# Kernel tuning notes

Hardware: AMD Instinct MI355X
Metric: run time of the kernel (lower is better)

## Reference

```python
import jax, jax.numpy as jnp
import numpy as np

# ---- multi-res 4D hash encoding config (Instant-NGP style) ----
L = 16                     # num_levels
T = 2 ** 19                # hash table entries per level (log2_hashmap_size)
FDIM = 2                   # features per entry (input_ch = L*2)
MIN_RES = np.array([16, 16, 16, 16], dtype=np.float64)
MAX_RES = np.array([256, 256, 256, 128], dtype=np.float64)
_growth = (MAX_RES / MIN_RES) ** (1.0 / (L - 1))
RES = np.floor(MIN_RES[None, :] * _growth[None, :] ** np.arange(L)[:, None]).astype(np.int32)  # [L,4]
PRIMES = np.array([1, 2654435761, 805459861, 3674653429], dtype=np.uint32)
# 16 corner offsets of the 4D hypercube
OFFS = np.array([[(c >> d) & 1 for d in range(4)] for c in range(16)], dtype=np.int32)  # [16,4]


def hash_encode(x, table):
    """x: [N,4] in [0,1); table: [L,T,FDIM] -> [N, L*FDIM]."""
    offs = jnp.asarray(OFFS)
    primes = jnp.asarray(PRIMES)
    outs = []
    for l in range(L):  # fixed small loop over levels
        res = jnp.asarray(RES[l], dtype=x.dtype)          # [4]
        pos = x * (res - 1.0)                              # [N,4]
        base = jnp.floor(pos)
        frac = pos - base                                  # [N,4]
        base_i = base.astype(jnp.int32)
        coord = jnp.clip(base_i[:, None, :] + offs[None], 0, jnp.asarray(RES[l] - 1))  # [N,16,4]
        h = coord.astype(jnp.uint32) * primes              # [N,16,4] u32 wraparound mult
        idx = (h[..., 0] ^ h[..., 1] ^ h[..., 2] ^ h[..., 3]) & jnp.uint32(T - 1)      # [N,16]
        feats = table[l][idx.astype(jnp.int32)]            # irregular gather -> [N,16,FDIM]
        # quadrilinear weights: prod over dims of frac / (1-frac)
        w = jnp.prod(jnp.where(offs[None] == 1, frac[:, None, :], 1.0 - frac[:, None, :]), axis=-1)  # [N,16]
        outs.append(jnp.einsum('nc,ncf->nf', w, feats))    # [N,FDIM]
    return jnp.concatenate(outs, axis=-1)                  # [N, L*FDIM]


def setup_inputs() -> dict:
    key = jax.random.key(0)
    ks = jax.random.split(key, 8)
    N = 1048576
    H = 64
    in_ch = L * FDIM  # 32
    x = jax.random.uniform(ks[0], (N, 4), dtype=jnp.float32)
    # NGP hash tables initialized uniform in [-1e-4, 1e-4]
    table = jax.random.uniform(ks[1], (L, T, FDIM), dtype=jnp.float32, minval=-1e-4, maxval=1e-4)
    def lin(k, out_d, in_d):
        b = 1.0 / np.sqrt(in_d)
        return jax.random.uniform(k, (out_d, in_d), dtype=jnp.float32, minval=-b, maxval=b)
    w0 = lin(ks[2], H, in_ch)
    w1 = lin(ks[3], H, H)
    w2 = lin(ks[4], H, H)
    w_out = lin(ks[5], 3, H)
    b_out = jax.random.uniform(ks[6], (3,), dtype=jnp.float32, minval=-1.0/np.sqrt(H), maxval=1.0/np.sqrt(H))
    return {"x": x, "table": table, "w0": w0, "w1": w1, "w2": w2, "w_out": w_out, "b_out": b_out}


def reference(x, table, w0, w1, w2, w_out, b_out):
    h = hash_encode(x, table)                 # [N, 32]
    for W in (w0, w1, w2):                    # bias-free Linear + ReLU x3
        h = jax.nn.relu(h @ W.T)
    v = h @ w_out.T + b_out                   # [N, 3]
    return v
```

## Files before the change

kernel.cpp:

```cpp
#include <hip/hip_runtime.h>
#include <math.h>

#define NLVL  16
#define TSZ   (1u << 19)
#define TMASK (TSZ - 1u)

struct ResArr { int m1[NLVL * 4]; };

typedef short  short8  __attribute__((ext_vector_type(8)));
typedef float  float4v __attribute__((ext_vector_type(4)));

static __device__ __forceinline__ unsigned short f2bf(float f) {
    unsigned u = __float_as_uint(f);
    return (unsigned short)((u + 0x7fffu + ((u >> 16) & 1u)) >> 16);
}

__global__ __launch_bounds__(256, 4)
void ingp_encode(const float4* __restrict__ x,
                 const float2* __restrict__ table,
                 unsigned*     __restrict__ featbf,
                 int N, int chunksPerLevel, ResArr res)
{
    const int l     = blockIdx.x / chunksPerLevel;
    const int chunk = blockIdx.x - l * chunksPerLevel;
    const int n     = chunk * 256 + threadIdx.x;
    if (n >= N) return;

    const float4 xv = x[n];
    const float px[4] = {xv.x, xv.y, xv.z, xv.w};

    int   bi[4];
    float fr[4], om[4];
    #pragma unroll
    for (int d = 0; d < 4; ++d) {
        const int r = res.m1[l * 4 + d];
        const float pos = px[d] * (float)r;
        const float fb  = floorf(pos);
        fr[d] = pos - fb;
        om[d] = 1.0f - fr[d];
        bi[d] = (int)fb;
    }
    const float2* tl  = table + (size_t)l * TSZ;
    const float4* tl4 = (const float4*)tl;

    unsigned hrest[8];
    #pragma unroll
    for (int p = 0; p < 8; ++p) {
        const int c1 = bi[1] + ( p       & 1);
        const int c2 = bi[2] + ((p >> 1) & 1);
        const int c3 = bi[3] + ((p >> 2) & 1);
        hrest[p] = ((unsigned)c1 * 2654435761u)
                 ^ ((unsigned)c2 * 805459861u)
                 ^ ((unsigned)c3 * 3674653429u);
    }

    float2 fv[16];
    if ((bi[0] & 1) == 0) {
        #pragma unroll
        for (int p = 0; p < 8; ++p) {
            const unsigned h = ((unsigned)bi[0] ^ hrest[p]) & TMASK;
            const float4 q = tl4[h >> 1];
            const bool odd = (h & 1);
            fv[2 * p]     = odd ? make_float2(q.z, q.w) : make_float2(q.x, q.y);
            fv[2 * p + 1] = odd ? make_float2(q.x, q.y) : make_float2(q.z, q.w);
        }
    } else {
        #pragma unroll
        for (int p = 0; p < 8; ++p) {
            const unsigned hA = ((unsigned)bi[0]       ^ hrest[p]) & TMASK;
            const unsigned hB = ((unsigned)(bi[0] + 1) ^ hrest[p]) & TMASK;
            fv[2 * p]     = tl[hA];
            fv[2 * p + 1] = tl[hB];
        }
    }

    float wt[16];
    #pragma unroll
    for (int c = 0; c < 16; ++c) {
        float w = ( c       & 1) ? fr[0] : om[0];
        w      *= ((c >> 1) & 1) ? fr[1] : om[1];
        w      *= ((c >> 2) & 1) ? fr[2] : om[2];
        w      *= ((c >> 3) & 1) ? fr[3] : om[3];
        wt[c] = w;
    }

    float a0 = 0.0f, a1 = 0.0f;
    #pragma unroll
    for (int c = 0; c < 16; ++c) {
        a0 = fmaf(wt[c], fv[c].x, a0);
        a1 = fmaf(wt[c], fv[c].y, a1);
    }
    featbf[(size_t)l * N + n] = (unsigned)f2bf(a0) | ((unsigned)f2bf(a1) << 16);
}

#define TILE_BODY(P0, A0)                                                     \
{                                                                             \
    float4v acc0[4];                                                          \
    _Pragma("unroll")                                                         \
    for (int t = 0; t < 4; ++t) {                                             \
        acc0[t] = (float4v){0.f, 0.f, 0.f, 0.f};                              \
        acc0[t] = __builtin_amdgcn_mfma_f32_16x16x32_bf16(A0, w0f[t], acc0[t], 0, 0, 0); \
    }                                                                         \
    _Pragma("unroll")                                                         \
    for (int t = 0; t < 4; ++t)                                               \
        _Pragma("unroll")                                                     \
        for (int r = 0; r < 4; ++r)                                           \
            *(unsigned short*)(hbase + (q * 4 + r) * 144 + (t * 16 + nn) * 2) = \
                f2bf(fmaxf(acc0[t][r], 0.0f));                                \
    short8 a1[2];                                                             \
    _Pragma("unroll")                                                         \
    for (int s = 0; s < 2; ++s)                                               \
        a1[s] = *(const short8*)(hbase + nn * 144 + s * 64 + q * 16);         \
    float4v acc1[4];                                                          \
    _Pragma("unroll")                                                         \
    for (int t = 0; t < 4; ++t) {                                             \
        acc1[t] = (float4v){0.f, 0.f, 0.f, 0.f};                              \
        _Pragma("unroll")                                                     \
        for (int s = 0; s < 2; ++s)                                           \
            acc1[t] = __builtin_amdgcn_mfma_f32_16x16x32_bf16(a1[s], w1f[s][t], acc1[t], 0, 0, 0); \
    }                                                                         \
    _Pragma("unroll")                                                         \
    for (int t = 0; t < 4; ++t)                                               \
        _Pragma("unroll")                                                     \
        for (int r = 0; r < 4; ++r)                                           \
            *(unsigned short*)(hbase + (q * 4 + r) * 144 + (t * 16 + nn) * 2) = \
                f2bf(fmaxf(acc1[t][r], 0.0f));                                \
    short8 a2[2];                                                             \
    _Pragma("unroll")                                                         \
    for (int s = 0; s < 2; ++s)                                               \
        a2[s] = *(const short8*)(hbase + nn * 144 + s * 64 + q * 16);         \
    float4v acc2[4];                                                          \
    _Pragma("unroll")                                                         \
    for (int t = 0; t < 4; ++t) {                                             \
        acc2[t] = (float4v){0.f, 0.f, 0.f, 0.f};                              \
        _Pragma("unroll")                                                     \
        for (int s = 0; s < 2; ++s)                                           \
            acc2[t] = __builtin_amdgcn_mfma_f32_16x16x32_bf16(a2[s], w2f[s][t], acc2[t], 0, 0, 0); \
    }                                                                         \
    _Pragma("unroll")                                                         \
    for (int t = 0; t < 4; ++t)                                               \
        _Pragma("unroll")                                                     \
        for (int r = 0; r < 4; ++r)                                           \
            *(unsigned short*)(hbase + (q * 4 + r) * 144 + (t * 16 + nn) * 2) = \
                f2bf(fmaxf(acc2[t][r], 0.0f));                                \
    short8 a3[2];                                                             \
    _Pragma("unroll")                                                         \
    for (int s = 0; s < 2; ++s)                                               \
        a3[s] = *(const short8*)(hbase + nn * 144 + s * 64 + q * 16);         \
    float4v oc = (float4v){0.f, 0.f, 0.f, 0.f};                               \
    _Pragma("unroll")                                                         \
    for (int s = 0; s < 2; ++s)                                               \
        oc = __builtin_amdgcn_mfma_f32_16x16x32_bf16(a3[s], wof[s], oc, 0, 0, 0); \
    if (nn < 3) {                                                             \
        _Pragma("unroll")                                                     \
        for (int r = 0; r < 4; ++r) {                                         \
            const int pt = (P0) + q * 4 + r;                                  \
            if (pt < N) out[pt * 3 + nn] = oc[r] + bias;                      \
        }                                                                     \
    }                                                                         \
}

__global__ __launch_bounds__(256, 2)
void ingp_mlp_mfma(const unsigned* __restrict__ featbf,
                   const float*    __restrict__ w0,
                   const float*    __restrict__ w1,
                   const float*    __restrict__ w2,
                   const float*    __restrict__ wout,
                   const float*    __restrict__ bout,
                   float*          __restrict__ out,
                   int N, int tilesPerWave)
{
    __shared__ char lds_raw[4 * 16 * 144];
    const int tid  = threadIdx.x;
    const int wave = tid >> 6;
    const int lane = tid & 63;
    const int q    = lane >> 4;
    const int nn   = lane & 15;
    char* hbase = lds_raw + wave * (16 * 144);

    short8 w0f[4];
    #pragma unroll
    for (int t = 0; t < 4; ++t) {
        const float* wr = w0 + (t * 16 + nn) * 32 + q * 8;
        #pragma unroll
        for (int e = 0; e < 8; ++e) w0f[t][e] = (short)f2bf(wr[e]);
    }
    short8 w1f[2][4], w2f[2][4];
    #pragma unroll
    for (int s = 0; s < 2; ++s) {
        #pragma unroll
        for (int t = 0; t < 4; ++t) {
            const float* wr1 = w1 + (t * 16 + nn) * 64 + s * 32 + q * 8;
            const float* wr2 = w2 + (t * 16 + nn) * 64 + s * 32 + q * 8;
            #pragma unroll
            for (int e = 0; e < 8; ++e) {
                w1f[s][t][e] = (short)f2bf(wr1[e]);
                w2f[s][t][e] = (short)f2bf(wr2[e]);
            }
        }
    }
    short8 wof[2];
    #pragma unroll
    for (int s = 0; s < 2; ++s) {
        #pragma unroll
        for (int e = 0; e < 8; ++e) {
            wof[s][e] = (nn < 3) ? (short)f2bf(wout[nn * 64 + s * 32 + q * 8 + e])
                                 : (short)0;
        }
    }
    const float bias = (nn < 3) ? bout[nn] : 0.0f;

    const int waveId = blockIdx.x * 4 + wave;
    const int base   = waveId * tilesPerWave;

    unsigned ufA[4], ufB[4];
    {
        const int pA = (base * 16 < N) ? (base * 16 + nn) : 0;
        const int pB = ((base + 1) * 16 < N) ? ((base + 1) * 16 + nn) : 0;
        #pragma unroll
        for (int v = 0; v < 4; ++v) {
            ufA[v] = featbf[(size_t)(q * 4 + v) * N + pA];
            ufB[v] = featbf[(size_t)(q * 4 + v) * N + pB];
        }
    }

    for (int it = 0; it < tilesPerWave; it += 2) {
        const int p0A = (base + it) * 16;
        if (p0A >= N) break;

        short8 a0A;
        #pragma unroll
        for (int v = 0; v < 4; ++v) {
            a0A[2 * v]     = (short)(ufA[v] & 0xffffu);
            a0A[2 * v + 1] = (short)(ufA[v] >> 16);
        }
        {
            const int p0n = (base + it + 2) * 16;
            const bool more = (it + 2 < tilesPerWave) && (p0n < N);
            const int pn = more ? (p0n + nn) : 0;
            #pragma unroll
            for (int v = 0; v < 4; ++v)
                ufA[v] = featbf[(size_t)(q * 4 + v) * N + pn];
        }
        TILE_BODY(p0A, a0A)

        const int p0B = (base + it + 1) * 16;
        if (p0B < N && it + 1 < tilesPerWave) {
            short8 a0B;
            #pragma unroll
            for (int v = 0; v < 4; ++v) {
                a0B[2 * v]     = (short)(ufB[v] & 0xffffu);
                a0B[2 * v + 1] = (short)(ufB[v] >> 16);
            }
            {
                const int p0n = (base + it + 3) * 16;
                const bool more = (it + 3 < tilesPerWave) && (p0n < N);
                const int pn = more ? (p0n + nn) : 0;
                #pragma unroll
                for (int v = 0; v < 4; ++v)
                    ufB[v] = featbf[(size_t)(q * 4 + v) * N + pn];
            }
            TILE_BODY(p0B, a0B)
        }
    }
}

__global__ __launch_bounds__(256, 2)
void ingp_fused(const float4* __restrict__ x,
                const float2* __restrict__ table,
                const float*  __restrict__ w0,
                const float*  __restrict__ w1,
                const float*  __restrict__ w2,
                const float*  __restrict__ wout,
                const float*  __restrict__ bout,
                float*        __restrict__ out,
                int N, ResArr res)
{
    const int n = blockIdx.x * blockDim.x + threadIdx.x;
    if (n >= N) return;

    const float4 xv = x[n];
    const float px[4] = {xv.x, xv.y, xv.z, xv.w};

    float h1[64];
    #pragma unroll
    for (int j = 0; j < 64; ++j) h1[j] = 0.0f;

    float a0p = 0.0f, a1p = 0.0f;

    #pragma unroll 1
    for (int l = 0; l < NLVL; ++l) {
        int   rm[4], bi[4];
        float fr[4], om[4];
        #pragma unroll
        for (int d = 0; d < 4; ++d) {
            const int r = res.m1[l * 4 + d];
            rm[d] = r;
            const float pos = px[d] * (float)r;
            const float fb  = floorf(pos);
            fr[d] = pos - fb;
            om[d] = 1.0f - fr[d];
            bi[d] = (int)fb;
        }
        const float2* tl = table + (size_t)l * TSZ;

        float2 fv[16];
        float  wt[16];
        #pragma unroll
        for (int c = 0; c < 16; ++c) {
            int c0 = bi[0] + ( c       & 1);
            int c1 = bi[1] + ((c >> 1) & 1);
            int c2 = bi[2] + ((c >> 2) & 1);
            int c3 = bi[3] + ((c >> 3) & 1);
            c0 = min(max(c0, 0), rm[0]);
            c1 = min(max(c1, 0), rm[1]);
            c2 = min(max(c2, 0), rm[2]);
            c3 = min(max(c3, 0), rm[3]);
            const unsigned hh = (unsigned)c0
                              ^ ((unsigned)c1 * 2654435761u)
                              ^ ((unsigned)c2 * 805459861u)
                              ^ ((unsigned)c3 * 3674653429u);
            fv[c] = tl[hh & TMASK];
            float w = ( c       & 1) ? fr[0] : om[0];
            w      *= ((c >> 1) & 1) ? fr[1] : om[1];
            w      *= ((c >> 2) & 1) ? fr[2] : om[2];
            w      *= ((c >> 3) & 1) ? fr[3] : om[3];
            wt[c] = w;
        }
        {
            const int lp = (l == 0) ? 0 : (l - 1);
            const float* w0c = w0 + 2 * lp;
            #pragma unroll
            for (int j = 0; j < 64; ++j)
                h1[j] = fmaf(w0c[j * 32], a0p, fmaf(w0c[j * 32 + 1], a1p, h1[j]));
        }
        float a0 = 0.0f, a1 = 0.0f;
        #pragma unroll
        for (int c = 0; c < 16; ++c) {
            a0 = fmaf(wt[c], fv[c].x, a0);
            a1 = fmaf(wt[c], fv[c].y, a1);
        }
        a0p = a0; a1p = a1;
    }
    {
        const float* w0c = w0 + 2 * (NLVL - 1);
        #pragma unroll
        for (int j = 0; j < 64; ++j)
            h1[j] = fmaf(w0c[j * 32], a0p, fmaf(w0c[j * 32 + 1], a1p, h1[j]));
    }
    #pragma unroll
    for (int j = 0; j < 64; ++j) h1[j] = fmaxf(h1[j], 0.0f);

    float h2[64];
    #pragma unroll
    for (int j = 0; j < 64; ++j) {
        float acc = 0.0f;
        const float* wr = w1 + j * 64;
        #pragma unroll
        for (int i = 0; i < 64; ++i) acc = fmaf(wr[i], h1[i], acc);
        h2[j] = fmaxf(acc, 0.0f);
    }
    float h3[64];
    #pragma unroll
    for (int j = 0; j < 64; ++j) {
        float acc = 0.0f;
        const float* wr = w2 + j * 64;
        #pragma unroll
        for (int i = 0; i < 64; ++i) acc = fmaf(wr[i], h2[i], acc);
        h3[j] = fmaxf(acc, 0.0f);
    }
    float o[3];
    #pragma unroll
    for (int k = 0; k < 3; ++k) {
        float acc = bout[k];
        const float* wr = wout + k * 64;
        #pragma unroll
        for (int i = 0; i < 64; ++i) acc = fmaf(wr[i], h3[i], acc);
        o[k] = acc;
    }
    out[n * 3 + 0] = o[0];
    out[n * 3 + 1] = o[1];
    out[n * 3 + 2] = o[2];
}

extern "C" void kernel_launch(void* const* d_in, const int* in_sizes, int n_in,
                              void* d_out, int out_size, void* d_ws, size_t ws_size,
                              hipStream_t stream) {
    (void)n_in; (void)out_size;

    const float* x     = (const float*)d_in[0];
    const float* table = (const float*)d_in[1];
    const float* w0    = (const float*)d_in[2];
    const float* w1    = (const float*)d_in[3];
    const float* w2    = (const float*)d_in[4];
    const float* wout  = (const float*)d_in[5];
    const float* bout  = (const float*)d_in[6];
    float* out = (float*)d_out;

    const int N = in_sizes[0] / 4;

    ResArr res;
    for (int d = 0; d < 4; ++d) {
        const double minr = 16.0;
        const double maxr = (d == 3) ? 128.0 : 256.0;
        const double growth = pow(maxr / minr, 1.0 / (double)(NLVL - 1));
        for (int l = 0; l < NLVL; ++l) {
            const int r = (int)floor(minr * pow(growth, (double)l));
            res.m1[l * 4 + d] = r - 1;
        }
    }

    const size_t featBytes = (size_t)NLVL * (size_t)N * sizeof(unsigned);
    const int chunksPerLevel = (N + 255) / 256;

    if (ws_size >= featBytes) {
        unsigned* featbf = (unsigned*)d_ws;
        hipLaunchKernelGGL(ingp_encode, dim3(NLVL * chunksPerLevel), dim3(256),
                           0, stream, (const float4*)x, (const float2*)table,
                           featbf, N, chunksPerLevel, res);

        const int tilesPerWave = 8;
        const int tiles  = (N + 15) / 16;
        const int waves  = (tiles + tilesPerWave - 1) / tilesPerWave;
        const int blocks = (waves + 3) / 4;
        hipLaunchKernelGGL(ingp_mlp_mfma, dim3(blocks), dim3(256), 0, stream,
                           featbf, w0, w1, w2, wout, bout, out, N, tilesPerWave);
    } else {
        hipLaunchKernelGGL(ingp_fused, dim3((N + 255) / 256), dim3(256), 0, stream,
                           (const float4*)x, (const float2*)table,
                           w0, w1, w2, wout, bout, out, N, res);
    }
}
```

Before: 837.8 us.

## Overlap MLP on first 3/4 of points with encoding of last quarter

Splits the point range into two parts. The first part is encoded alone. A combined kernel then interleaves MLP blocks for that part with encode blocks for the remainder, and a final MLP kernel handles the rest. The goal is to fill the GPU with compute-bound MFMA work while the gather-bound hash encoding runs, hiding the idle time at the boundary between the two stages. Block roles are picked from the block index, and nothing explicitly checks that feature writes finish before the MLP blocks read them. Correctness therefore depends on kernel launch order.

```diff
diff --git a/kernel.cpp b/kernel.cpp
--- a/kernel.cpp
+++ b/kernel.cpp
@@ -15,15 +15,12 @@
     return (unsigned short)((u + 0x7fffu + ((u >> 16) & 1u)) >> 16);
 }
 
-__global__ __launch_bounds__(256, 4)
-void ingp_encode(const float4* __restrict__ x,
-                 const float2* __restrict__ table,
-                 unsigned*     __restrict__ featbf,
-                 int N, int chunksPerLevel, ResArr res)
+static __device__ __forceinline__
+void encode_point(const float4* __restrict__ x,
+                  const float2* __restrict__ table,
+                  unsigned*     __restrict__ featbf,
+                  int N, int l, int n, const ResArr& res)
 {
-    const int l     = blockIdx.x / chunksPerLevel;
-    const int chunk = blockIdx.x - l * chunksPerLevel;
-    const int n     = chunk * 256 + threadIdx.x;
     if (n >= N) return;
 
     const float4 xv = x[n];
@@ -91,6 +88,17 @@
         a1 = fmaf(wt[c], fv[c].y, a1);
     }
     featbf[(size_t)l * N + n] = (unsigned)f2bf(a0) | ((unsigned)f2bf(a1) << 16);
+}
+
+__global__ __launch_bounds__(256, 4)
+void ingp_encode(const float4* __restrict__ x,
+                 const float2* __restrict__ table,
+                 unsigned*     __restrict__ featbf,
+                 int N, int pointBase, int chunksPerLevel, ResArr res)
+{
+    const int l     = blockIdx.x / chunksPerLevel;
+    const int chunk = blockIdx.x - l * chunksPerLevel;
+    encode_point(x, table, featbf, N, l, pointBase + chunk * 256 + (int)threadIdx.x, res);
 }
 
 #define TILE_BODY(P0, A0)                                                     \
@@ -160,6 +168,109 @@
     }                                                                         \
 }
 
+static __device__ __forceinline__
+void mlp_block_body(const unsigned* __restrict__ featbf,
+                    const float*    __restrict__ w0,
+                    const float*    __restrict__ w1,
+                    const float*    __restrict__ w2,
+                    const float*    __restrict__ wout,
+                    const float*    __restrict__ bout,
+                    float*          __restrict__ out,
+                    int N, int firstTile, char* lds_raw)
+{
+    const int tid  = (int)threadIdx.x;
+    const int wave = tid >> 6;
+    const int lane = tid & 63;
+    const int q    = lane >> 4;
+    const int nn   = lane & 15;
+    char* hbase = lds_raw + wave * (16 * 144);
+
+    short8 w0f[4];
+    #pragma unroll
+    for (int t = 0; t < 4; ++t) {
+        const float* wr = w0 + (t * 16 + nn) * 32 + q * 8;
+        #pragma unroll
+        for (int e = 0; e < 8; ++e) w0f[t][e] = (short)f2bf(wr[e]);
+    }
+    short8 w1f[2][4], w2f[2][4];
+    #pragma unroll
+    for (int s = 0; s < 2; ++s) {
+        #pragma unroll
+        for (int t = 0; t < 4; ++t) {
+            const float* wr1 = w1 + (t * 16 + nn) * 64 + s * 32 + q * 8;
+            const float* wr2 = w2 + (t * 16 + nn) * 64 + s * 32 + q * 8;
+            #pragma unroll
+            for (int e = 0; e < 8; ++e) {
+                w1f[s][t][e] = (short)f2bf(wr1[e]);
+                w2f[s][t][e] = (short)f2bf(wr2[e]);
+            }
+        }
+    }
+    short8 wof[2];
+    #pragma unroll
+    for (int s = 0; s < 2; ++s) {
+        #pragma unroll
+        for (int e = 0; e < 8; ++e) {
+            wof[s][e] = (nn < 3) ? (short)f2bf(wout[nn * 64 + s * 32 + q * 8 + e])
+                                 : (short)0;
+        }
+    }
+    const float bias = (nn < 3) ? bout[nn] : 0.0f;
+
+    const int base = firstTile + wave * 8;
+
+    unsigned ufA[4], ufB[4];
+    {
+        const int pA = (base * 16 < N) ? (base * 16 + nn) : 0;
+        const int pB = ((base + 1) * 16 < N) ? ((base + 1) * 16 + nn) : 0;
+        #pragma unroll
+        for (int v = 0; v < 4; ++v) {
+            ufA[v] = featbf[(size_t)(q * 4 + v) * N + pA];
+            ufB[v] = featbf[(size_t)(q * 4 + v) * N + pB];
+        }
+    }
+
+    for (int it = 0; it < 8; it += 2) {
+        const int p0A = (base + it) * 16;
+        if (p0A >= N) break;
+
+        short8 a0A;
+        #pragma unroll
+        for (int v = 0; v < 4; ++v) {
+            a0A[2 * v]     = (short)(ufA[v] & 0xffffu);
+            a0A[2 * v + 1] = (short)(ufA[v] >> 16);
+        }
+        {
+            const int p0n = (base + it + 2) * 16;
+            const bool more = (it + 2 < 8) && (p0n < N);
+            const int pn = more ? (p0n + nn) : 0;
+            #pragma unroll
+            for (int v = 0; v < 4; ++v)
+                ufA[v] = featbf[(size_t)(q * 4 + v) * N + pn];
+        }
+        TILE_BODY(p0A, a0A)
+
+        const int p0B = (base + it + 1) * 16;
+        if (p0B < N) {
+            short8 a0B;
+            #pragma unroll
+            for (int v = 0; v < 4; ++v) {
+                a0B[2 * v]     = (short)(ufB[v] & 0xffffu);
+                a0B[2 * v + 1] = (short)(ufB[v] >> 16);
+            }
+            {
+                const int p0n = (base + it + 3) * 16;
+                const bool more = (it + 3 < 8) && (p0n < N);
+                const int pn = more ? (p0n + nn) : 0;
+                #pragma unroll
+                for (int v = 0; v < 4; ++v)
+                    ufB[v] = featbf[(size_t)(q * 4 + v) * N + pn];
+            }
+            TILE_BODY(p0B, a0B)
+        }
+    }
+}
+
 __global__ __launch_bounds__(256, 2)
 void ingp_mlp_mfma(const unsigned* __restrict__ featbf,
                    const float*    __restrict__ w0,
@@ -168,100 +279,39 @@
                    const float*    __restrict__ wout,
                    const float*    __restrict__ bout,
                    float*          __restrict__ out,
-                   int N, int tilesPerWave)
+                   int N, int firstTileBase)
 {
     __shared__ char lds_raw[4 * 16 * 144];
-    const int tid  = threadIdx.x;
-    const int wave = tid >> 6;
-    const int lane = tid & 63;
-    const int q    = lane >> 4;
-    const int nn   = lane & 15;
-    char* hbase = lds_raw + wave * (16 * 144);
-
-    short8 w0f[4];
-    #pragma unroll
-    for (int t = 0; t < 4; ++t) {
-        const float* wr = w0 + (t * 16 + nn) * 32 + q * 8;
-        #pragma unroll
-        for (int e = 0; e < 8; ++e) w0f[t][e] = (short)f2bf(wr[e]);
-    }
-    short8 w1f[2][4], w2f[2][4];
-    #pragma unroll
-    for (int s = 0; s < 2; ++s) {
-        #pragma unroll
-        for (int t = 0; t < 4; ++t) {
-            const float* wr1 = w1 + (t * 16 + nn) * 64 + s * 32 + q * 8;
-            const float* wr2 = w2 + (t * 16 + nn) * 64 + s * 32 + q * 8;
-            #pragma unroll
-            for (int e = 0; e < 8; ++e) {
-                w1f[s][t][e] = (short)f2bf(wr1[e]);
-                w2f[s][t][e] = (short)f2bf(wr2[e]);
-            }
-        }
-    }
-    short8 wof[2];
-    #pragma unroll
-    for (int s = 0; s < 2; ++s) {
-        #pragma unroll
-        for (int e = 0; e < 8; ++e) {
-            wof[s][e] = (nn < 3) ? (short)f2bf(wout[nn * 64 + s * 32 + q * 8 + e])
-                                 : (short)0;
-        }
-    }
-    const float bias = (nn < 3) ? bout[nn] : 0.0f;
-
-    const int waveId = blockIdx.x * 4 + wave;
-    const int base   = waveId * tilesPerWave;
-
-    unsigned ufA[4], ufB[4];
-    {
-        const int pA = (base * 16 < N) ? (base * 16 + nn) : 0;
-        const int pB = ((base + 1) * 16 < N) ? ((base + 1) * 16 + nn) : 0;
-        #pragma unroll
-        for (int v = 0; v < 4; ++v) {
-            ufA[v] = featbf[(size_t)(q * 4 + v) * N + pA];
-            ufB[v] = featbf[(size_t)(q * 4 + v) * N + pB];
-        }
-    }
-
-    for (int it = 0; it < tilesPerWave; it += 2) {
-        const int p0A = (base + it) * 16;
-        if (p0A >= N) break;
-
-        short8 a0A;
-        #pragma unroll
-        for (int v = 0; v < 4; ++v) {
-            a0A[2 * v]     = (short)(ufA[v] & 0xffffu);
-            a0A[2 * v + 1] = (short)(ufA[v] >> 16);
-        }
-        {
-            const int p0n = (base + it + 2) * 16;
-            const bool more = (it + 2 < tilesPerWave) && (p0n < N);
-            const int pn = more ? (p0n + nn) : 0;
-            #pragma unroll
-            for (int v = 0; v < 4; ++v)
-                ufA[v] = featbf[(size_t)(q * 4 + v) * N + pn];
-        }
-        TILE_BODY(p0A, a0A)
-
-        const int p0B = (base + it + 1) * 16;
-        if (p0B < N && it + 1 < tilesPerWave) {
-            short8 a0B;
-            #pragma unroll
-            for (int v = 0; v < 4; ++v) {
-                a0B[2 * v]     = (short)(ufB[v] & 0xffffu);
-                a0B[2 * v + 1] = (short)(ufB[v] >> 16);
-            }
-            {
-                const int p0n = (base + it + 3) * 16;
-                const bool more = (it + 3 < tilesPerWave) && (p0n < N);
-                const int pn = more ? (p0n + nn) : 0;
-                #pragma unroll
-                for (int v = 0; v < 4; ++v)
-                    ufB[v] = featbf[(size_t)(q * 4 + v) * N + pn];
-            }
-            TILE_BODY(p0B, a0B)
-        }
+    mlp_block_body(featbf, w0, w1, w2, wout, bout, out, N,
+                   firstTileBase + (int)blockIdx.x * 32, lds_raw);
+}
+
+__global__ __launch_bounds__(256, 2)
+void ingp_pipe(const float4* __restrict__ x,
+               const float2* __restrict__ table,
+               unsigned*     __restrict__ featbf,
+               const float*  __restrict__ w0,
+               const float*  __restrict__ w1,
+               const float*  __restrict__ w2,
+               const float*  __restrict__ wout,
+               const float*  __restrict__ bout,
+               float*        __restrict__ out,
+               int N, int pointBaseE, int chunksPerLevelB, int MB, int G,
+               ResArr res)
+{
+    __shared__ char lds_raw[4 * 16 * 144];
+    const int b = (int)blockIdx.x;
+    const long long t0 = (long long)b * MB;
+    const int mlow  = (int)(t0 / G);
+    const int mhigh = (int)((t0 + MB) / G);
+    if (mhigh > mlow) {
+        mlp_block_body(featbf, w0, w1, w2, wout, bout, out, N, mlow * 32, lds_raw);
+    } else {
+        const int e     = b - mlow;
+        const int l     = e / chunksPerLevelB;
+        const int chunk = e - l * chunksPerLevelB;
+        encode_point(x, table, featbf, N, l,
+                     pointBaseE + chunk * 256 + (int)threadIdx.x, res);
     }
 }
 
@@ -411,20 +461,44 @@
     }
 
     const size_t featBytes = (size_t)NLVL * (size_t)N * sizeof(unsigned);
-    const int chunksPerLevel = (N + 255) / 256;
 
     if (ws_size >= featBytes) {
         unsigned* featbf = (unsigned*)d_ws;
-        hipLaunchKernelGGL(ingp_encode, dim3(NLVL * chunksPerLevel), dim3(256),
-                           0, stream, (const float4*)x, (const float2*)table,
-                           featbf, N, chunksPerLevel, res);
-
-        const int tilesPerWave = 8;
-        const int tiles  = (N + 15) / 16;
-        const int waves  = (tiles + tilesPerWave - 1) / tilesPerWave;
-        const int blocks = (waves + 3) / 4;
-        hipLaunchKernelGGL(ingp_mlp_mfma, dim3(blocks), dim3(256), 0, stream,
-                           featbf, w0, w1, w2, wout, bout, out, N, tilesPerWave);
+
+        const int A = (int)((((long long)N * 3) / 4) / 512 * 512);
+        const bool pipe_ok = (N % 256 == 0) && (A > 0) && (A < N);
+
+        if (pipe_ok) {
+            const int chunksA = A / 256;
+            hipLaunchKernelGGL(ingp_encode, dim3(NLVL * chunksA), dim3(256),
+                               0, stream, (const float4*)x, (const float2*)table,
+                               featbf, N, 0, chunksA, res);
+
+            const int chunksB = (N - A) / 256;
+            const int EB = NLVL * chunksB;
+            const int MB = A / 512;
+            const int G  = EB + MB;
+            hipLaunchKernelGGL(ingp_pipe, dim3(G), dim3(256), 0, stream,
+                               (const float4*)x, (const float2*)table, featbf,
+                               w0, w1, w2, wout, bout, out,
+                               N, A, chunksB, MB, G, res);
+
+            const int tilesB  = (N - A + 15) / 16;
+            const int wavesB  = (tilesB + 7) / 8;
+            const int blocksB = (wavesB + 3) / 4;
+            hipLaunchKernelGGL(ingp_mlp_mfma, dim3(blocksB), dim3(256), 0, stream,
+                               featbf, w0, w1, w2, wout, bout, out, N, A / 16);
+        } else {
+            const int chunksPerLevel = (N + 255) / 256;
+            hipLaunchKernelGGL(ingp_encode, dim3(NLVL * chunksPerLevel), dim3(256),
+                               0, stream, (const float4*)x, (const float2*)table,
+                               featbf, N, 0, chunksPerLevel, res);
+            const int tiles  = (N + 15) / 16;
+            const int waves  = (tiles + 7) / 8;
+            const int blocks = (waves + 3) / 4;
+            hipLaunchKernelGGL(ingp_mlp_mfma, dim3(blocks), dim3(256), 0, stream,
+                               featbf, w0, w1, w2, wout, bout, out, N, 0);
+        }
     } else {
         hipLaunchKernelGGL(ingp_fused, dim3((N + 255) / 256), dim3(256), 0, stream,
                            (const float4*)x, (const float2*)table,
```

Result: slower. 876.2 us (+4.6%).

## Convert hash table to bf16 each call and gather packed bf16 entries

Applied to the files above, without the earlier changes.

Adds a pre-pass kernel that converts the fp32 hash table into packed bf16 pairs in workspace. The encode kernel then gathers 4-byte entries instead of 8-byte ones, and for odd base coordinates it uses 16-byte aligned quad loads to fetch both neighbours at once. This halves the footprint of the random gathers so more of the table stays in cache, at the cost of a full-table conversion pass (16M floats read) on every call and reduced precision of the table values. The MLP kernel is refactored into a helper with the tile count fixed at 8.

```diff
diff --git a/kernel.cpp b/kernel.cpp
--- a/kernel.cpp
+++ b/kernel.cpp
@@ -15,15 +15,23 @@
     return (unsigned short)((u + 0x7fffu + ((u >> 16) & 1u)) >> 16);
 }
 
-__global__ __launch_bounds__(256, 4)
-void ingp_encode(const float4* __restrict__ x,
-                 const float2* __restrict__ table,
-                 unsigned*     __restrict__ featbf,
-                 int N, int chunksPerLevel, ResArr res)
-{
-    const int l     = blockIdx.x / chunksPerLevel;
-    const int chunk = blockIdx.x - l * chunksPerLevel;
-    const int n     = chunk * 256 + threadIdx.x;
+__global__ __launch_bounds__(256)
+void cvt_table(const float4* __restrict__ t, uint2* __restrict__ o, int totalPairs)
+{
+    for (int i = blockIdx.x * 256 + (int)threadIdx.x; i < totalPairs;
+         i += gridDim.x * 256) {
+        const float4 e = t[i];
+        o[i] = make_uint2((unsigned)f2bf(e.x) | ((unsigned)f2bf(e.y) << 16),
+                          (unsigned)f2bf(e.z) | ((unsigned)f2bf(e.w) << 16));
+    }
+}
+
+static __device__ __forceinline__
+void encode_point_bf16(const float4*   __restrict__ x,
+                       const unsigned* __restrict__ tbl,
+                       unsigned*       __restrict__ featbf,
+                       int N, int l, int n, const ResArr& res)
+{
     if (n >= N) return;
 
     const float4 xv = x[n];
@@ -40,8 +48,9 @@
         om[d] = 1.0f - fr[d];
         bi[d] = (int)fb;
     }
-    const float2* tl  = table + (size_t)l * TSZ;
-    const float4* tl4 = (const float4*)tl;
+    const unsigned* tl  = tbl + (size_t)l * TSZ;
+    const uint2*    tl2 = (const uint2*)tl;
+    const uint4*    tl4 = (const uint4*)tl;
 
     unsigned hrest[8];
     #pragma unroll
@@ -54,6 +63,115 @@
                  ^ ((unsigned)c3 * 3674653429u);
     }
 
+    const int b0 = bi[0];
+    unsigned ea[8], eb[8];
+
+    if ((b0 & 1) == 0) {
+        #pragma unroll
+        for (int p = 0; p < 8; ++p) {
+            const unsigned h = ((unsigned)b0 ^ hrest[p]) & TMASK;
+            const uint2 q = tl2[h >> 1];
+            ea[p] = (h & 1u) ? q.y : q.x;
+            eb[p] = (h & 1u) ? q.x : q.y;
+        }
+    } else if ((b0 & 3) == 1) {
+        #pragma unroll
+        for (int p = 0; p < 8; ++p) {
+            const unsigned hA = ((unsigned)b0 ^ hrest[p]) & TMASK;
+            const uint4 q = tl4[hA >> 2];
+            const unsigned jA  = hA & 3u;
+            const unsigned loA = (jA & 2u) ? q.z : q.x;
+            const unsigned hiA = (jA & 2u) ? q.w : q.y;
+            const unsigned loB = (jA & 2u) ? q.x : q.z;
+            const unsigned hiB = (jA & 2u) ? q.y : q.w;
+            ea[p] = (jA & 1u) ? hiA : loA;
+            eb[p] = (jA & 1u) ? loB : hiB;
+        }
+    } else {
+        #pragma unroll
+        for (int p = 0; p < 8; ++p) {
+            const unsigned hA = ((unsigned)b0       ^ hrest[p]) & TMASK;
+            const unsigned hB = ((unsigned)(b0 + 1) ^ hrest[p]) & TMASK;
+            ea[p] = tl[hA];
+            eb[p] = tl[hB];
+        }
+    }
+
+    float2 fv[16];
+    #pragma unroll
+    for (int p = 0; p < 8; ++p) {
+        fv[2 * p]     = make_float2(__uint_as_float(ea[p] << 16),
+                                    __uint_as_float(ea[p] & 0xffff0000u));
+        fv[2 * p + 1] = make_float2(__uint_as_float(eb[p] << 16),
+                                    __uint_as_float(eb[p] & 0xffff0000u));
+    }
+
+    float wt[16];
+    #pragma unroll
+    for (int c = 0; c < 16; ++c) {
+        float w = ( c       & 1) ? fr[0] : om[0];
+        w      *= ((c >> 1) & 1) ? fr[1] : om[1];
+        w      *= ((c >> 2) & 1) ? fr[2] : om[2];
+        w      *= ((c >> 3) & 1) ? fr[3] : om[3];
+        wt[c] = w;
+    }
+
+    float a0 = 0.0f, a1 = 0.0f;
+    #pragma unroll
+    for (int c = 0; c < 16; ++c) {
+        a0 = fmaf(wt[c], fv[c].x, a0);
+        a1 = fmaf(wt[c], fv[c].y, a1);
+    }
+    featbf[(size_t)l * N + n] = (unsigned)f2bf(a0) | ((unsigned)f2bf(a1) << 16);
+}
+
+__global__ __launch_bounds__(256, 4)
+void ingp_encode_bf16(const float4*   __restrict__ x,
+                      const unsigned* __restrict__ tbl,
+                      unsigned*       __restrict__ featbf,
+                      int N, int chunksPerLevel, ResArr res)
+{
+    const int l     = blockIdx.x / chunksPerLevel;
+    const int chunk = blockIdx.x - l * chunksPerLevel;
+    encode_point_bf16(x, tbl, featbf, N, l, chunk * 256 + (int)threadIdx.x, res);
+}
+
+static __device__ __forceinline__
+void encode_point_f32(const float4* __restrict__ x,
+                      const float2* __restrict__ table,
+                      unsigned*     __restrict__ featbf,
+                      int N, int l, int n, const ResArr& res)
+{
+    if (n >= N) return;
+
+    const float4 xv = x[n];
+    const float px[4] = {xv.x, xv.y, xv.z, xv.w};
+
+    int   bi[4];
+    float fr[4], om[4];
+    #pragma unroll
+    for (int d = 0; d < 4; ++d) {
+        const int r = res.m1[l * 4 + d];
+        const float pos = px[d] * (float)r;
+        const float fb  = floorf(pos);
+        fr[d] = pos - fb;
+        om[d] = 1.0f - fr[d];
+        bi[d] = (int)fb;
+    }
+    const float2* tl  = table + (size_t)l * TSZ;
+    const float4* tl4 = (const float4*)tl;
+
+    unsigned hrest[8];
+    #pragma unroll
+    for (int p = 0; p < 8; ++p) {
+        const int c1 = bi[1] + ( p       & 1);
+        const int c2 = bi[2] + ((p >> 1) & 1);
+        const int c3 = bi[3] + ((p >> 2) & 1);
+        hrest[p] = ((unsigned)c1 * 2654435761u)
+                 ^ ((unsigned)c2 * 805459861u)
+                 ^ ((unsigned)c3 * 3674653429u);
+    }
+
     float2 fv[16];
     if ((bi[0] & 1) == 0) {
         #pragma unroll
@@ -91,6 +209,17 @@
         a1 = fmaf(wt[c], fv[c].y, a1);
     }
     featbf[(size_t)l * N + n] = (unsigned)f2bf(a0) | ((unsigned)f2bf(a1) << 16);
+}
+
+__global__ __launch_bounds__(256, 4)
+void ingp_encode_f32(const float4* __restrict__ x,
+                     const float2* __restrict__ table,
+                     unsigned*     __restrict__ featbf,
+                     int N, int chunksPerLevel, ResArr res)
+{
+    const int l     = blockIdx.x / chunksPerLevel;
+    const int chunk = blockIdx.x - l * chunksPerLevel;
+    encode_point_f32(x, table, featbf, N, l, chunk * 256 + (int)threadIdx.x, res);
 }
 
 #define TILE_BODY(P0, A0)                                                     \
@@ -160,6 +289,109 @@
     }                                                                         \
 }
 
+static __device__ __forceinline__
+void mlp_block_body(const unsigned* __restrict__ featbf,
+                    const float*    __restrict__ w0,
+                    const float*    __restrict__ w1,
+                    const float*    __restrict__ w2,
+                    const float*    __restrict__ wout,
+                    const float*    __restrict__ bout,
+                    float*          __restrict__ out,
+                    int N, int firstTile, char* lds_raw)
+{
+    const int tid  = (int)threadIdx.x;
+    const int wave = tid >> 6;
+    const int lane = tid & 63;
+    const int q    = lane >> 4;
+    const int nn   = lane & 15;
+    char* hbase = lds_raw + wave * (16 * 144);
+
+    short8 w0f[4];
+    #pragma unroll
+    for (int t = 0; t < 4; ++t) {
+        const float* wr = w0 + (t * 16 + nn) * 32 + q * 8;
+        #pragma unroll
+        for (int e = 0; e < 8; ++e) w0f[t][e] = (short)f2bf(wr[e]);
+    }
+    short8 w1f[2][4], w2f[2][4];
+    #pragma unroll
+    for (int s = 0; s < 2; ++s) {
+        #pragma unroll
+        for (int t = 0; t < 4; ++t) {
+            const float* wr1 = w1 + (t * 16 + nn) * 64 + s * 32 + q * 8;
+            const float* wr2 = w2 + (t * 16 + nn) * 64 + s * 32 + q * 8;
+            #pragma unroll
+            for (int e = 0; e < 8; ++e) {
+                w1f[s][t][e] = (short)f2bf(wr1[e]);
+                w2f[s][t][e] = (short)f2bf(wr2[e]);
+            }
+        }
+    }
+    short8 wof[2];
+    #pragma unroll
+    for (int s = 0; s < 2; ++s) {
+        #pragma unroll
+        for (int e = 0; e < 8; ++e) {
+            wof[s][e] = (nn < 3) ? (short)f2bf(wout[nn * 64 + s * 32 + q * 8 + e])
+                                 : (short)0;
+        }
+    }
+    const float bias = (nn < 3) ? bout[nn] : 0.0f;
+
+    const int base = firstTile + wave * 8;
+
+    unsigned ufA[4], ufB[4];
+    {
+        const int pA = (base * 16 < N) ? (base * 16 + nn) : 0;
+        const int pB = ((base + 1) * 16 < N) ? ((base + 1) * 16 + nn) : 0;
+        #pragma unroll
+        for (int v = 0; v < 4; ++v) {
+            ufA[v] = featbf[(size_t)(q * 4 + v) * N + pA];
+            ufB[v] = featbf[(size_t)(q * 4 + v) * N + pB];
+        }
+    }
+
+    for (int it = 0; it < 8; it += 2) {
+        const int p0A = (base + it) * 16;
+        if (p0A >= N) break;
+
+        short8 a0A;
+        #pragma unroll
+        for (int v = 0; v < 4; ++v) {
+            a0A[2 * v]     = (short)(ufA[v] & 0xffffu);
+            a0A[2 * v + 1] = (short)(ufA[v] >> 16);
+        }
+        {
+            const int p0n = (base + it + 2) * 16;
+            const bool more = (it + 2 < 8) && (p0n < N);
+            const int pn = more ? (p0n + nn) : 0;
+            #pragma unroll
+            for (int v = 0; v < 4; ++v)
+                ufA[v] = featbf[(size_t)(q * 4 + v) * N + pn];
+        }
+        TILE_BODY(p0A, a0A)
+
+        const int p0B = (base + it + 1) * 16;
+        if (p0B < N) {
+            short8 a0B;
+            #pragma unroll
+            for (int v = 0; v < 4; ++v) {
+                a0B[2 * v]     = (short)(ufB[v] & 0xffffu);
+                a0B[2 * v + 1] = (short)(ufB[v] >> 16);
+            }
+            {
+                const int p0n = (base + it + 3) * 16;
+                const bool more = (it + 3 < 8) && (p0n < N);
+                const int pn = more ? (p0n + nn) : 0;
+                #pragma unroll
+                for (int v = 0; v < 4; ++v)
+                    ufB[v] = featbf[(size_t)(q * 4 + v) * N + pn];
+            }
+            TILE_BODY(p0B, a0B)
+        }
+    }
+}
+
 __global__ __launch_bounds__(256, 2)
 void ingp_mlp_mfma(const unsigned* __restrict__ featbf,
                    const float*    __restrict__ w0,
@@ -168,101 +400,11 @@
                    const float*    __restrict__ wout,
                    const float*    __restrict__ bout,
                    float*          __restrict__ out,
-                   int N, int tilesPerWave)
+                   int N)
 {
     __shared__ char lds_raw[4 * 16 * 144];
-    const int tid  = threadIdx.x;
-    const int wave = tid >> 6;
-    const int lane = tid & 63;
-    const int q    = lane >> 4;
-    const int nn   = lane & 15;
-    char* hbase = lds_raw + wave * (16 * 144);
-
-    short8 w0f[4];
-    #pragma unroll
-    for (int t = 0; t < 4; ++t) {
-        const float* wr = w0 + (t * 16 + nn) * 32 + q * 8;
-        #pragma unroll
-        for (int e = 0; e < 8; ++e) w0f[t][e] = (short)f2bf(wr[e]);
-    }
-    short8 w1f[2][4], w2f[2][4];
-    #pragma unroll
-    for (int s = 0; s < 2; ++s) {
-        #pragma unroll
-        for (int t = 0; t < 4; ++t) {
-            const float* wr1 = w1 + (t * 16 + nn) * 64 + s * 32 + q * 8;
-            const float* wr2 = w2 + (t * 16 + nn) * 64 + s * 32 + q * 8;
-            #pragma unroll
-            for (int e = 0; e < 8; ++e) {
-                w1f[s][t][e] = (short)f2bf(wr1[e]);
-                w2f[s][t][e] = (short)f2bf(wr2[e]);
-            }
-        }
-    }
-    short8 wof[2];
-    #pragma unroll
-    for (int s = 0; s < 2; ++s) {
-        #pragma unroll
-        for (int e = 0; e < 8; ++e) {
-            wof[s][e] = (nn < 3) ? (short)f2bf(wout[nn * 64 + s * 32 + q * 8 + e])
-                                 : (short)0;
-        }
-    }
-    const float bias = (nn < 3) ? bout[nn] : 0.0f;
-
-    const int waveId = blockIdx.x * 4 + wave;
-    const int base   = waveId * tilesPerWave;
-
-    unsigned ufA[4], ufB[4];
-    {
-        const int pA = (base * 16 < N) ? (base * 16 + nn) : 0;
-        const int pB = ((base + 1) * 16 < N) ? ((base + 1) * 16 + nn) : 0;
-        #pragma unroll
-        for (int v = 0; v < 4; ++v) {
-            ufA[v] = featbf[(size_t)(q * 4 + v) * N + pA];
-            ufB[v] = featbf[(size_t)(q * 4 + v) * N + pB];
-        }
-    }
-
-    for (int it = 0; it < tilesPerWave; it += 2) {
-        const int p0A = (base + it) * 16;
-        if (p0A >= N) break;
-
-        short8 a0A;
-        #pragma unroll
-        for (int v = 0; v < 4; ++v) {
-            a0A[2 * v]     = (short)(ufA[v] & 0xffffu);
-            a0A[2 * v + 1] = (short)(ufA[v] >> 16);
-        }
-        {
-            const int p0n = (base + it + 2) * 16;
-            const bool more = (it + 2 < tilesPerWave) && (p0n < N);
-            const int pn = more ? (p0n + nn) : 0;
-            #pragma unroll
-            for (int v = 0; v < 4; ++v)
-                ufA[v] = featbf[(size_t)(q * 4 + v) * N + pn];
-        }
-        TILE_BODY(p0A, a0A)
-
-        const int p0B = (base + it + 1) * 16;
-        if (p0B < N && it + 1 < tilesPerWave) {
-            short8 a0B;
-            #pragma unroll
-            for (int v = 0; v < 4; ++v) {
-                a0B[2 * v]     = (short)(ufB[v] & 0xffffu);
-                a0B[2 * v + 1] = (short)(ufB[v] >> 16);
-            }
-            {
-                const int p0n = (base + it + 3) * 16;
-                const bool more = (it + 3 < tilesPerWave) && (p0n < N);
-                const int pn = more ? (p0n + nn) : 0;
-                #pragma unroll
-                for (int v = 0; v < 4; ++v)
-                    ufB[v] = featbf[(size_t)(q * 4 + v) * N + pn];
-            }
-            TILE_BODY(p0B, a0B)
-        }
-    }
+    mlp_block_body(featbf, w0, w1, w2, wout, bout, out, N,
+                   (int)blockIdx.x * 32, lds_raw);
 }
 
 __global__ __launch_bounds__(256, 2)
@@ -410,21 +552,38 @@
         }
     }
 
+    const size_t tblBytes  = (size_t)NLVL * TSZ * sizeof(unsigned);
     const size_t featBytes = (size_t)NLVL * (size_t)N * sizeof(unsigned);
     const int chunksPerLevel = (N + 255) / 256;
 
-    if (ws_size >= featBytes) {
+    if (ws_size >= tblBytes + featBytes) {
+        unsigned* tblbf  = (unsigned*)d_ws;
+        unsigned* featbf = (unsigned*)((char*)d_ws + tblBytes);
+
+        hipLaunchKernelGGL(cvt_table, dim3(2048), dim3(256), 0, stream,
+                           (const float4*)table, (uint2*)tblbf,
+                           (int)(NLVL * TSZ / 2));
+
+        hipLaunchKernelGGL(ingp_encode_bf16, dim3(NLVL * chunksPerLevel), dim3(256),
+                           0, stream, (const float4*)x, tblbf,
+                           featbf, N, chunksPerLevel, res);
+
+        const int tiles  = (N + 15) / 16;
+        const int waves  = (tiles + 7) / 8;
+        const int blocks = (waves + 3) / 4;
+        hipLaunchKernelGGL(ingp_mlp_mfma, dim3(blocks), dim3(256), 0, stream,
+                           featbf, w0, w1, w2, wout, bout, out, N);
+    } else if (ws_size >= featBytes) {
         unsigned* featbf = (unsigned*)d_ws;
-        hipLaunchKernelGGL(ingp_encode, dim3(NLVL * chunksPerLevel), dim3(256),
+        hipLaunchKernelGGL(ingp_encode_f32, dim3(NLVL * chunksPerLevel), dim3(256),
                            0, stream, (const float4*)x, (const float2*)table,
                            featbf, N, chunksPerLevel, res);
 
-        const int tilesPerWave = 8;
         const int tiles  = (N + 15) / 16;
-        const int waves  = (tiles + tilesPerWave - 1) / tilesPerWave;
+        const int waves  = (tiles + 7) / 8;
         const int blocks = (waves + 3) / 4;
         hipLaunchKernelGGL(ingp_mlp_mfma, dim3(blocks), dim3(256), 0, stream,
-                           featbf, w0, w1, w2, wout, bout, out, N, tilesPerWave);
+                           featbf, w0, w1, w2, wout, bout, out, N);
     } else {
         hipLaunchKernelGGL(ingp_fused, dim3((N + 255) / 256), dim3(256), 0, stream,
                            (const float4*)x, (const float2*)table,
```

Measured after the change: 746.0 us. 11.0% less time.
